# Kernel optimization log

Measured on AMD Instinct MI355X. Metric: run time of the kernel, lower is better.

Reference implementation:

```python
import jax, jax.numpy as jnp
import numpy as np

B, P, C = 32, 8732, 21
TOP_K = 200
CONF_THRESH = 0.01
NMS_THRESH = 0.45
VAR0, VAR1 = 0.1, 0.2  # VOC PRIOR_BOX VARIANCE


def setup_inputs() -> dict:
    key = jax.random.key(0)
    k1, k2, k3 = jax.random.split(key, 3)
    loc_data = jax.random.normal(k1, (B, P, 4), jnp.float32)
    conf_data = jax.random.uniform(k2, (B, P, C), jnp.float32)
    prior_data = jax.random.uniform(k3, (P, 4), jnp.float32)
    return {"loc_data": loc_data, "conf_data": conf_data, "prior_data": prior_data}


def _decode(loc, priors):
    # priors are (cx, cy, w, h); returns (x1, y1, x2, y2)
    cxcy = priors[:, :2] + loc[:, :2] * VAR0 * priors[:, 2:]
    wh = priors[:, 2:] * jnp.exp(loc[:, 2:] * VAR1)
    x1y1 = cxcy - wh * 0.5
    return jnp.concatenate([x1y1, x1y1 + wh], axis=1)  # [P,4]


def _nms_class(boxes, scores):
    # boxes [P,4], scores [P] -> [TOP_K,5] rows of (score, x1, y1, x2, y2)
    s = jnp.where(scores > CONF_THRESH, scores, -1.0)
    top_s, idx = jax.lax.top_k(s, TOP_K)          # descending scores
    b = boxes[idx]                                 # [K,4]
    valid = top_s > CONF_THRESH
    x1, y1, x2, y2 = b[:, 0], b[:, 1], b[:, 2], b[:, 3]
    area = (x2 - x1) * (y2 - y1)
    # pairwise intersection / IoU [K,K]
    xx1 = jnp.maximum(x1[:, None], x1[None, :])
    yy1 = jnp.maximum(y1[:, None], y1[None, :])
    xx2 = jnp.minimum(x2[:, None], x2[None, :])
    yy2 = jnp.minimum(y2[:, None], y2[None, :])
    inter = jnp.clip(xx2 - xx1, 0.0) * jnp.clip(yy2 - yy1, 0.0)
    union = area[:, None] + area[None, :] - inter
    iou = inter / union
    ar = jnp.arange(TOP_K)

    def step(carry, j):
        kept, suppressed = carry
        is_kept = valid[j] & ~suppressed[j]
        kept = kept.at[j].set(is_kept)
        suppressed = suppressed | (is_kept & (iou[j] > NMS_THRESH) & (ar > j))
        return (kept, suppressed), None

    (kept, _), _ = jax.lax.scan(
        step, (jnp.zeros(TOP_K, bool), jnp.zeros(TOP_K, bool)), ar)
    # compact kept rows to the front (matches output[i, cl, :count] = ...)
    pos = jnp.cumsum(kept) - 1
    safe = jnp.where(kept, pos, TOP_K)
    rows = jnp.concatenate([top_s[:, None], b], axis=1)  # [K,5]
    out = jnp.zeros((TOP_K + 1, 5), rows.dtype).at[safe].set(rows)[:TOP_K]
    return out


def reference(loc_data, conf_data, prior_data):
    def per_image(loc, conf):
        boxes = _decode(loc, prior_data)           # [P,4]
        return jax.vmap(lambda s: _nms_class(boxes, s), in_axes=1)(conf)  # [C,K,5]

    out = jax.vmap(per_image)(loc_data, conf_data)  # [B,C,K,5]
    return out.at[:, 0].set(0.0)  # class 0 (background) is skipped in original
```

## Files before the change

kernel.cpp:

```cpp
#include <hip/hip_runtime.h>
#include <stdint.h>

#define B_ 32
#define P_ 8732
#define PPAD 8736
#define C_ 21
#define TOPK 200
#define TGT 228
#define CONF_T 0.01f
#define NMS_T 0.45f
#define NCH2 35
#define NT 512
#define KV4 5

__device__ __forceinline__ uint32_t f2s(float f) {
    uint32_t u = __float_as_uint(f);
    return (u & 0x80000000u) ? ~u : (u | 0x80000000u);
}
__device__ __forceinline__ float s2f(uint32_t s) {
    uint32_t b = (s & 0x80000000u) ? (s & 0x7FFFFFFFu) : ~s;
    return __uint_as_float(b);
}

__global__ __launch_bounds__(256) void transpose_keys(const float* __restrict__ conf,
                                                      uint32_t* __restrict__ keys) {
    const int b = blockIdx.x / NCH2;
    const int ch = blockIdx.x % NCH2;
    const int p0 = ch * 256;
    const int n = min(256, P_ - p0);
    const int tid = threadIdx.x;
    __shared__ float tile[256 * C_];
    const float* src = conf + ((size_t)b * P_ + p0) * C_;
    const int tot = n * C_;
    for (int i = tid; i < tot; i += 256) tile[i] = src[i];
    __syncthreads();
    uint32_t* dst = keys + (size_t)b * C_ * PPAD + p0;
    if (tid < n) {
        #pragma unroll
        for (int c = 0; c < C_; ++c) {
            float v = tile[tid * C_ + c];
            v = (v > CONF_T) ? v : -1.0f;
            dst[(size_t)c * PPAD + tid] = f2s(v);
        }
    }
    if (ch == NCH2 - 1 && tid >= n && tid < n + (PPAD - P_)) {
        #pragma unroll
        for (int c = 0; c < C_; ++c) dst[(size_t)c * PPAD + tid] = 0u;
    }
}

template<bool RAW>
__global__ __launch_bounds__(NT, 6) void detect_kernel(
    const float* __restrict__ loc, const float* __restrict__ prior,
    const uint32_t* __restrict__ keys, const float* __restrict__ conf,
    float* __restrict__ out)
{
    const int task = blockIdx.x;
    const int b = task / C_;
    const int c = task % C_;
    const int tid = threadIdx.x;
    const int lane = tid & 63;
    float* outp = out + (size_t)task * TOPK * 5;

    if (c == 0) {
        for (int e = tid; e < TOPK * 5; e += NT) outp[e] = 0.0f;
        return;
    }

    __shared__ uint64_t cand[256];
    __shared__ float4 bbox[TOPK];
    __shared__ float bar[TOPK], bs[TOPK];
    __shared__ unsigned long long msk[TOPK * 4];
    __shared__ unsigned long long vmask[4];
    __shared__ int order[TOPK];
    __shared__ int s_cnt, s_nk;
    __shared__ int s_c2[2];

    uint4 kv[KV4];
    if (!RAW) {
        const uint4* kp = (const uint4*)(keys + (size_t)task * PPAD);
        #pragma unroll
        for (int r = 0; r < KV4; ++r) {
            int q = tid + r * NT;
            kv[r] = (q < PPAD / 4) ? kp[q] : make_uint4(0u, 0u, 0u, 0u);
        }
    } else {
        const float* sp = conf + (size_t)b * P_ * C_ + c;
        #pragma unroll
        for (int r = 0; r < KV4; ++r) {
            uint32_t uu[4];
            #pragma unroll
            for (int c4 = 0; c4 < 4; ++c4) {
                int p = (tid + r * NT) * 4 + c4;
                if (p < P_) {
                    float v = sp[(size_t)p * C_];
                    v = (v > CONF_T) ? v : -1.0f;
                    uu[c4] = f2s(v);
                } else uu[c4] = 0u;
            }
            kv[r] = make_uint4(uu[0], uu[1], uu[2], uu[3]);
        }
    }

    if (tid == 0) s_cnt = 0;
    if (tid < 2) s_c2[tid] = 0;
    for (int i2 = tid; i2 < TOPK * 4; i2 += NT) msk[i2] = 0ull;
    __syncthreads();

    uint32_t lo = 0u, hi = 0xFFFFFFFFu;
    uint32_t t = f2s(1.0f - (float)TGT / (float)P_);
    uint32_t vthr = 0u;
    for (int it = 0; ; ++it) {
        const int slot = it & 1;
        int my = 0;
        #pragma unroll
        for (int r = 0; r < KV4; ++r)
            my += (kv[r].x >= t) + (kv[r].y >= t) + (kv[r].z >= t) + (kv[r].w >= t);
        #pragma unroll
        for (int d = 1; d < 64; d <<= 1) my += __shfl_down(my, d);
        if (lane == 0) atomicAdd(&s_c2[slot], my);
        __syncthreads();
        const int cnt = s_c2[slot];
        __syncthreads();
        if (tid == 0) s_c2[slot] = 0;
        if (cnt >= TOPK && cnt <= 256) { vthr = t; break; }
        if (cnt > 256) lo = t; else hi = t;
        if (hi - lo <= 1) { vthr = lo; break; }
        uint32_t tn = 0;
        bool bis = (it >= 8) || (cnt == 0);
        if (!bis) {
            const float sc = s2f(t);
            const float sn = 1.0f - (1.0f - sc) * (float)TGT / (float)cnt;
            tn = f2s(sn);
            if (!(tn > lo && tn < hi)) bis = true;
        }
        if (bis) tn = lo + ((hi - lo) >> 1);
        t = tn;
    }

    #pragma unroll
    for (int r = 0; r < KV4; ++r) {
        const int pb = (tid + r * NT) * 4;
        uint32_t uu[4] = {kv[r].x, kv[r].y, kv[r].z, kv[r].w};
        #pragma unroll
        for (int c4 = 0; c4 < 4; ++c4) {
            uint32_t u = uu[c4];
            if (u >= vthr) {
                int pos = atomicAdd(&s_cnt, 1);
                if (pos < 256) cand[pos] = ((uint64_t)u << 32) | (uint32_t)(~(uint32_t)(pb + c4));
            }
        }
    }
    __syncthreads();
    if (tid < 256 && tid >= s_cnt) cand[tid] = 0ull;
    __syncthreads();

    uint64_t v = (tid < 256) ? cand[tid] : 0ull;
    for (int kk = 2; kk <= 256; kk <<= 1) {
        for (int j = kk >> 1; j > 0; j >>= 1) {
            if (j >= 64) {
                __syncthreads();
                if (tid < 256) cand[tid] = v;
                __syncthreads();
                if (tid < 256) {
                    uint64_t pv = cand[tid ^ j];
                    bool keepmax = (((tid & j) == 0) == ((tid & kk) == 0));
                    v = keepmax ? (v > pv ? v : pv) : (v < pv ? v : pv);
                }
            } else if (tid < 256) {
                uint64_t pv = __shfl_xor(v, j);
                bool keepmax = (((tid & j) == 0) == ((tid & kk) == 0));
                v = keepmax ? (v > pv ? v : pv) : (v < pv ? v : pv);
            }
        }
    }

    float my_sc = -1.0f;
    if (tid < TOPK) {
        uint32_t su = (uint32_t)(v >> 32);
        int p = (int)(~(uint32_t)v);
        my_sc = s2f(su);
        const float4 l4 = *(const float4*)(loc + ((size_t)b * P_ + p) * 4);
        const float4 pr = *(const float4*)(prior + (size_t)p * 4);
        float cx = __fadd_rn(pr.x, __fmul_rn(__fmul_rn(l4.x, 0.1f), pr.z));
        float cy = __fadd_rn(pr.y, __fmul_rn(__fmul_rn(l4.y, 0.1f), pr.w));
        float ew = (float)exp((double)__fmul_rn(l4.z, 0.2f));
        float eh = (float)exp((double)__fmul_rn(l4.w, 0.2f));
        float w  = __fmul_rn(pr.z, ew);
        float h  = __fmul_rn(pr.w, eh);
        float x1 = __fsub_rn(cx, __fmul_rn(w, 0.5f));
        float y1 = __fsub_rn(cy, __fmul_rn(h, 0.5f));
        float x2 = __fadd_rn(x1, w);
        float y2 = __fadd_rn(y1, h);
        bs[tid] = my_sc;
        bbox[tid] = make_float4(x1, y1, x2, y2);
        bar[tid] = __fmul_rn(__fsub_rn(x2, x1), __fsub_rn(y2, y1));
    }
    {
        unsigned long long bm = __ballot(tid < TOPK && my_sc > CONF_T);
        if (lane == 0 && tid < 256) vmask[tid >> 6] = bm;
    }
    __syncthreads();

    if (tid < 500) {
        const int rp = tid / 5;
        const int s  = tid - rp * 5;
        #pragma unroll
        for (int pass = 0; pass < 2; ++pass) {
            const int j  = pass ? (199 - rp) : rp;
            const int i0 = j + 1 + s;
            const float4 bj = bbox[j];
            const float  aj = bar[j];
            for (int i = i0; i < TOPK; i += 5) {
                const float4 bi = bbox[i];
                float xx1 = fmaxf(bj.x, bi.x);
                float yy1 = fmaxf(bj.y, bi.y);
                float xx2 = fminf(bj.z, bi.z);
                float yy2 = fminf(bj.w, bi.w);
                float dx = fmaxf(__fsub_rn(xx2, xx1), 0.0f);
                float dy = fmaxf(__fsub_rn(yy2, yy1), 0.0f);
                float inter = __fmul_rn(dx, dy);
                if (inter > 0.0f) {
                    float uni = __fsub_rn(__fadd_rn(aj, bar[i]), inter);
                    float t45 = __fmul_rn(NMS_T, uni);
                    float mar = __fmul_rn(t45, 1e-6f);
                    bool sup;
                    if (inter > __fadd_rn(t45, mar)) sup = true;
                    else if (inter < __fsub_rn(t45, mar)) sup = false;
                    else sup = (inter / uni > NMS_T);
                    if (sup) atomicOr(&msk[j * 4 + (i >> 6)], 1ull << (i & 63));
                }
            }
        }
    }
    __syncthreads();

    if (tid < 64) {
        const int L = tid;
        auto or_reduce = [&](unsigned long long x) {
            #pragma unroll
            for (int d = 1; d < 64; d <<= 1) x |= __shfl_xor(x, d);
            return x;
        };
        unsigned long long s1 = 0, s2 = 0, s3 = 0;
        int nk = 0;
        #pragma unroll
        for (int w = 0; w < 4; ++w) {
            const int j = (w << 6) | L;
            unsigned long long r0 = 0, r1 = 0, r2 = 0, r3 = 0;
            if (j < TOPK) {
                const unsigned long long* mr = &msk[j * 4];
                r0 = mr[0]; r1 = mr[1]; r2 = mr[2]; r3 = mr[3];
            }
            const unsigned long long rself = (w == 0) ? r0 : (w == 1) ? r1
                                           : (w == 2) ? r2 : r3;
            unsigned long long sw = (w == 0) ? 0ull : (w == 1) ? s1
                                  : (w == 2) ? s2 : s3;
            unsigned long long alive = vmask[w] & ~sw;
            unsigned long long pm = 0;
            while (alive) {
                int jl = __ffsll(alive) - 1;
                if (L == 0) order[nk] = (w << 6) | jl;
                ++nk;
                sw |= __shfl(rself, jl);
                pm |= (1ull << jl);
                alive &= ~(sw | (1ull << jl));
            }
            if (pm) {
                const bool picked = (pm >> L) & 1ull;
                if (w == 0) {
                    s1 |= or_reduce(picked ? r1 : 0ull);
                    s2 |= or_reduce(picked ? r2 : 0ull);
                    s3 |= or_reduce(picked ? r3 : 0ull);
                } else if (w == 1) {
                    s2 |= or_reduce(picked ? r2 : 0ull);
                    s3 |= or_reduce(picked ? r3 : 0ull);
                } else if (w == 2) {
                    s3 |= or_reduce(picked ? r3 : 0ull);
                }
            }
        }
        if (L == 0) s_nk = nk;
    }
    __syncthreads();

    const int nk = s_nk;
    for (int e = tid; e < TOPK * 5; e += NT) {
        int r = e / 5;
        int f = e - r * 5;
        float val = 0.0f;
        if (r < nk) {
            int j = order[r];
            float4 bb = bbox[j];
            val = (f == 0) ? bs[j] : (f == 1) ? bb.x : (f == 2) ? bb.y
                : (f == 3) ? bb.z : bb.w;
        }
        outp[e] = val;
    }
}

extern "C" void kernel_launch(void* const* d_in, const int* in_sizes, int n_in,
                              void* d_out, int out_size, void* d_ws, size_t ws_size,
                              hipStream_t stream) {
    const float* loc   = (const float*)d_in[0];
    const float* conf  = (const float*)d_in[1];
    const float* prior = (const float*)d_in[2];
    float* out = (float*)d_out;

    const size_t need = (size_t)B_ * C_ * PPAD * sizeof(uint32_t);
    if (ws_size >= need) {
        uint32_t* keys = (uint32_t*)d_ws;
        transpose_keys<<<B_ * NCH2, 256, 0, stream>>>(conf, keys);
        detect_kernel<false><<<B_ * C_, NT, 0, stream>>>(loc, prior, keys, conf, out);
    } else {
        detect_kernel<true><<<B_ * C_, NT, 0, stream>>>(loc, prior, nullptr, conf, out);
    }
}
```

Baseline: 125.8 us.

## Vectorize key transpose with float4 loads and raise detect kernel to 640 threads

Rewrites the conf-to-key transpose so it uses float4 global loads and uint4 stores, with each thread handling four priors for a strided subset of classes instead of one prior across all 21 classes. The aim is fewer, wider memory transactions. The detect kernel grows from 512 to 640 threads, with matching changes to KV4, launch bounds and the IoU pair-split stride (5 to 6), to spread the pairwise IoU work over more threads. This risks register pressure and occupancy changes, and depends on the per-chunk element count being divisible by 4 and the tail padding still being written correctly.

```diff
diff --git a/kernel.cpp b/kernel.cpp
--- a/kernel.cpp
+++ b/kernel.cpp
@@ -10,8 +10,8 @@
 #define CONF_T 0.01f
 #define NMS_T 0.45f
 #define NCH2 35
-#define NT 512
-#define KV4 5
+#define NT 640
+#define KV4 4
 
 __device__ __forceinline__ uint32_t f2s(float f) {
     uint32_t u = __float_as_uint(f);
@@ -20,6 +20,9 @@
 __device__ __forceinline__ float s2f(uint32_t s) {
     uint32_t b = (s & 0x80000000u) ? (s & 0x7FFFFFFFu) : ~s;
     return __uint_as_float(b);
+}
+__device__ __forceinline__ uint32_t keyof(float v) {
+    return f2s((v > CONF_T) ? v : -1.0f);
 }
 
 __global__ __launch_bounds__(256) void transpose_keys(const float* __restrict__ conf,
@@ -30,27 +33,34 @@
     const int n = min(256, P_ - p0);
     const int tid = threadIdx.x;
     __shared__ float tile[256 * C_];
-    const float* src = conf + ((size_t)b * P_ + p0) * C_;
-    const int tot = n * C_;
-    for (int i = tid; i < tot; i += 256) tile[i] = src[i];
+    const float4* src4 = (const float4*)(conf + ((size_t)b * P_ + p0) * C_);
+    float4* tile4 = (float4*)tile;
+    const int tot4 = (n * C_) >> 2;
+    for (int i = tid; i < tot4; i += 256) tile4[i] = src4[i];
     __syncthreads();
     uint32_t* dst = keys + (size_t)b * C_ * PPAD + p0;
-    if (tid < n) {
-        #pragma unroll
-        for (int c = 0; c < C_; ++c) {
-            float v = tile[tid * C_ + c];
-            v = (v > CONF_T) ? v : -1.0f;
-            dst[(size_t)c * PPAD + tid] = f2s(v);
-        }
-    }
-    if (ch == NCH2 - 1 && tid >= n && tid < n + (PPAD - P_)) {
-        #pragma unroll
-        for (int c = 0; c < C_; ++c) dst[(size_t)c * PPAD + tid] = 0u;
+    const int pg = tid & 63;
+    const int cs = tid >> 6;
+    const int ng = n >> 2;
+    if (pg < ng) {
+        for (int c = cs; c < C_; c += 4) {
+            const float* tp = &tile[4 * pg * C_ + c];
+            uint4 k;
+            k.x = keyof(tp[0 * C_]);
+            k.y = keyof(tp[1 * C_]);
+            k.z = keyof(tp[2 * C_]);
+            k.w = keyof(tp[3 * C_]);
+            *(uint4*)(dst + (size_t)c * PPAD + 4 * pg) = k;
+        }
+    }
+    if (ch == NCH2 - 1 && pg == ng) {
+        for (int c = cs; c < C_; c += 4)
+            *(uint4*)(dst + (size_t)c * PPAD + 4 * pg) = make_uint4(0u, 0u, 0u, 0u);
     }
 }
 
 template<bool RAW>
-__global__ __launch_bounds__(NT, 6) void detect_kernel(
+__global__ __launch_bounds__(NT, 7) void detect_kernel(
     const float* __restrict__ loc, const float* __restrict__ prior,
     const uint32_t* __restrict__ keys, const float* __restrict__ conf,
     float* __restrict__ out)
@@ -202,16 +212,16 @@
     }
     __syncthreads();
 
-    if (tid < 500) {
-        const int rp = tid / 5;
-        const int s  = tid - rp * 5;
+    if (tid < 600) {
+        const int rp = tid / 6;
+        const int s  = tid - rp * 6;
         #pragma unroll
         for (int pass = 0; pass < 2; ++pass) {
             const int j  = pass ? (199 - rp) : rp;
             const int i0 = j + 1 + s;
             const float4 bj = bbox[j];
             const float  aj = bar[j];
-            for (int i = i0; i < TOPK; i += 5) {
+            for (int i = i0; i < TOPK; i += 6) {
                 const float4 bi = bbox[i];
                 float xx1 = fmaxf(bj.x, bi.x);
                 float yy1 = fmaxf(bj.y, bi.y);
```

Measured after the change: 153.3 us. +21.9%, slower.
